# Performance work log

Hardware: AMD Instinct MI355X
Metric: run time of the kernel (lower is better)

The kernel has to match this reference:

```python
import jax, jax.numpy as jnp
import numpy as np

B, S, T = 32, 512, 64
DENC = 1024   # encoder dim == dhid
DHID = 1024
DEMB = 512
V = 32000
NEG = 1e20


def setup_inputs() -> dict:
    key = jax.random.key(0)
    ks = jax.random.split(key, 13)
    u = lambda k, shape, a: jax.random.uniform(k, shape, jnp.float32, -a, a)
    klstm = 1.0 / np.sqrt(DHID)
    kproj = 1.0 / np.sqrt(DENC + DHID)
    return {
        "enc": jax.random.normal(ks[0], (B, S, DENC), jnp.float32),
        "inp_mask": jnp.ones((B, S), jnp.float32),
        "label": jax.random.randint(ks[1], (B, T), 0, V),
        "emb_w": jax.random.normal(ks[2], (V, DEMB), jnp.float32) * 0.02,
        "W_ih": u(ks[3], (4 * DHID, DENC + DEMB), klstm),
        "b_ih": u(ks[4], (4 * DHID,), klstm),
        "W_hh": u(ks[5], (4 * DHID, DHID), klstm),
        "b_hh": u(ks[6], (4 * DHID,), klstm),
        "proj_W": u(ks[7], (DEMB, DENC + DHID), kproj),
        "proj_b": u(ks[8], (DEMB,), kproj),
        "emb0": u(ks[9], (DEMB,), 0.1),
        "h0": u(ks[10], (DHID,), 0.1),
        "c0": u(ks[11], (DHID,), 0.1),
    }


def reference(enc, inp_mask, label, emb_w, W_ih, b_ih, W_hh, b_hh,
              proj_W, proj_b, emb0, h0, c0):
    batch = enc.shape[0]
    vocab = emb_w.shape[0]
    h = jnp.broadcast_to(h0, (batch, h0.shape[0]))
    c = jnp.broadcast_to(c0, (batch, c0.shape[0]))
    e = jnp.broadcast_to(emb0, (batch, emb0.shape[0]))
    neg_mask = (1.0 - inp_mask) * NEG  # [B, S]
    emb_T = jax.lax.stop_gradient(emb_w).T  # detached vocab projection

    def step(carry, label_t):
        h, c, e = carry
        # attention over encoder states keyed by h
        score = jnp.einsum('bsd,bd->bs', enc, h) - neg_mask
        attn = jax.nn.softmax(score, axis=1)
        ctx = jnp.einsum('bs,bsd->bd', attn, enc)  # [B, DENC]
        # LSTMCell (torch gate order: i, f, g, o)
        x = jnp.concatenate([ctx, e], axis=1)
        gates = x @ W_ih.T + b_ih + h @ W_hh.T + b_hh
        i, f, g, o = jnp.split(gates, 4, axis=1)
        c = jax.nn.sigmoid(f) * c + jax.nn.sigmoid(i) * jnp.tanh(g)
        h = jax.nn.sigmoid(o) * jnp.tanh(c)
        # project to embedding space, score against vocab
        p = jnp.concatenate([ctx, h], axis=1) @ proj_W.T + proj_b
        out = p @ emb_T  # [B, V]
        # teacher forcing: next input embedding from label
        word = jnp.clip(label_t, 0, vocab - 1)
        e = emb_w[word]
        return (h, c, e), out

    _, outs = jax.lax.scan(step, (h, c, e), label.T)  # outs: [T, B, V]
    return jnp.transpose(outs, (1, 0, 2))  # [B, T, V]
```

## Files before the change

kernel.cpp:

```cpp
#include <hip/hip_runtime.h>
#include <hip/hip_bf16.h>


#define B_   32
#define S_   512
#define T_   64
#define DENC 1024
#define DHID 1024
#define DEMB 512
#define V_   32000
#define KX   2560
#define KP   2048
#define NCH  32

using short8 = __attribute__((ext_vector_type(8))) short;
using f32x4  = __attribute__((ext_vector_type(4))) float;
typedef __hip_bfloat16 bf16;

__device__ __forceinline__ float sigmoidf_(float x) { return 1.0f / (1.0f + expf(-x)); }
__device__ __forceinline__ bf16 bhi(float x) { return __float2bfloat16(x); }
__device__ __forceinline__ bf16 blo(float x) {
    return __float2bfloat16(x - __bfloat162float(__float2bfloat16(x)));
}

#define MFMA(a, b, c) __builtin_amdgcn_mfma_f32_16x16x32_bf16((a), (b), (c), 0, 0, 0)
#define DOT4(a, b) fmaf((a).x, (b).x, fmaf((a).y, (b).y, fmaf((a).z, (b).z, (a).w * (b).w)))


__global__ void k_build_wg(const float* __restrict__ W_ih, const float* __restrict__ W_hh,
                           const float* __restrict__ b_ih, const float* __restrict__ b_hh,
                           bf16* __restrict__ Wh, bf16* __restrict__ Wl, float* __restrict__ bias) {
    int jp = blockIdx.x;
    int g = jp & 3, d = jp >> 2;
    int j = g * 1024 + d;
    const float* wi = W_ih + (size_t)j * 1536;
    const float* wh = W_hh + (size_t)j * 1024;
    bf16* dh = Wh + (size_t)jp * KX;
    bf16* dl = Wl + (size_t)jp * KX;
    for (int i = threadIdx.x; i < 1024; i += 256) { float v = wi[i];      dh[i] = bhi(v);        dl[i] = blo(v); }
    for (int i = threadIdx.x; i < 1024; i += 256) { float v = wh[i];      dh[1024+i] = bhi(v);   dl[1024+i] = blo(v); }
    for (int i = threadIdx.x; i < 512;  i += 256) { float v = wi[1024+i]; dh[2048+i] = bhi(v);   dl[2048+i] = blo(v); }
    if (threadIdx.x == 0) bias[jp] = b_ih[j] + b_hh[j];
}

__global__ void k_cvt(const float* __restrict__ src, bf16* __restrict__ dst, long n) {
    long i = (long)blockIdx.x * blockDim.x + threadIdx.x;
    long stride = (long)gridDim.x * blockDim.x;
    for (; i < n; i += stride) dst[i] = __float2bfloat16(src[i]);
}

__global__ void k_cvt_split(const float* __restrict__ src, bf16* __restrict__ dh,
                            bf16* __restrict__ dl, long n) {
    long i = (long)blockIdx.x * blockDim.x + threadIdx.x;
    long stride = (long)gridDim.x * blockDim.x;
    for (; i < n; i += stride) { float v = src[i]; dh[i] = bhi(v); dl[i] = blo(v); }
}

__global__ void k_init(const float* __restrict__ h0, const float* __restrict__ c0,
                       const float* __restrict__ emb0,
                       float* __restrict__ h, float* __restrict__ c,
                       bf16* __restrict__ Hh, bf16* __restrict__ Hl,
                       bf16* __restrict__ Xh_, bf16* __restrict__ Xl_) {
    int b = blockIdx.x;
    for (int d = threadIdx.x; d < 1024; d += 256) {
        float v = h0[d];
        h[b * 1024 + d] = v;
        c[b * 1024 + d] = c0[d];
        Hh[b * 1024 + d] = bhi(v);
        Hl[b * 1024 + d] = blo(v);
    }
    for (int d = threadIdx.x; d < 512; d += 256) {
        float v = emb0[d];
        Xh_[(size_t)b * KX + 2048 + d] = bhi(v);
        Xl_[(size_t)b * KX + 2048 + d] = blo(v);
    }
}


__global__ __launch_bounds__(256) void k_att(
    const float* __restrict__ enc, const float* __restrict__ mask,
    const float* __restrict__ h,
    bf16* __restrict__ Xh_, bf16* __restrict__ Xl_,
    const bf16* __restrict__ Hh, const bf16* __restrict__ Hl,
    const bf16* __restrict__ PWh, const bf16* __restrict__ PWl,
    const float* __restrict__ pb, const float* __restrict__ emb_w,
    const int* __restrict__ label,
    bf16* __restrict__ Ph, bf16* __restrict__ Pl,
    float* __restrict__ pml, float* __restrict__ pctx, int t)
{
    __shared__ float pr[4][32][17];
    __shared__ float lctx[4][1024];
    __shared__ float lm[4], ll[4];

    int bid = blockIdx.x;
    int tid = threadIdx.x, wave = tid >> 6, lane = tid & 63;

    if (bid < 32) {
        if (t == 0) return;
        int tp = t - 1;
        int nb = bid * 16;
        int ncol = nb + (lane & 15);
        int kc = wave * 512;
        const short* ah;
        const short* al;
        size_t astr, aoff;
        if (wave < 2) { ah = (const short*)Xh_; al = (const short*)Xl_; astr = KX;   aoff = kc; }
        else          { ah = (const short*)Hh;  al = (const short*)Hl;  astr = 1024; aoff = kc - 1024; }
        const short* wrh = (const short*)PWh + (size_t)ncol * KP + kc + (lane >> 4) * 8;
        const short* wrl = (const short*)PWl + (size_t)ncol * KP + kc + (lane >> 4) * 8;
        size_t arow0 = (size_t)(lane & 15) * astr + aoff + (lane >> 4) * 8;
        size_t arow1 = (size_t)((lane & 15) + 16) * astr + aoff + (lane >> 4) * 8;
        f32x4 acc0 = {0, 0, 0, 0}, acc1 = {0, 0, 0, 0};
#pragma unroll 4
        for (int kk = 0; kk < 16; ++kk) {
            int ko = kk * 32;
            short8 a0h = *(const short8*)(ah + arow0 + ko);
            short8 a1h = *(const short8*)(ah + arow1 + ko);
            short8 a0l = *(const short8*)(al + arow0 + ko);
            short8 a1l = *(const short8*)(al + arow1 + ko);
            short8 bh = *(const short8*)(wrh + ko);
            short8 bl = *(const short8*)(wrl + ko);
            acc0 = MFMA(a0h, bh, acc0); acc1 = MFMA(a1h, bh, acc1);
            acc0 = MFMA(a0h, bl, acc0); acc1 = MFMA(a1h, bl, acc1);
            acc0 = MFMA(a0l, bh, acc0); acc1 = MFMA(a1l, bh, acc1);
        }
#pragma unroll
        for (int r = 0; r < 4; ++r) {
            pr[wave][(lane >> 4) * 4 + r][lane & 15]      = acc0[r];
            pr[wave][16 + (lane >> 4) * 4 + r][lane & 15] = acc1[r];
        }
        __syncthreads();
        for (int p = tid; p < 512; p += 256) {
            int bb = p >> 4, col = p & 15;
            float v = pr[0][bb][col] + pr[1][bb][col] + pr[2][bb][col] + pr[3][bb][col]
                      + pb[nb + col];
            size_t mi = (size_t)(bb * 64 + tp) * 512 + nb + col;
            Ph[mi] = bhi(v);
            Pl[mi] = blo(v);
        }
        int b = bid;
        int wd = label[b * 64 + tp];
        wd = wd < 0 ? 0 : (wd > V_ - 1 ? V_ - 1 : wd);
        const float* ew = emb_w + (size_t)wd * 512;
        for (int d = tid; d < 512; d += 256) {
            float v = ew[d];
            Xh_[(size_t)b * KX + 2048 + d] = bhi(v);
            Xl_[(size_t)b * KX + 2048 + d] = blo(v);
        }
        return;
    }

    if (t >= T_) return;
    int ab = bid - 32;
    int b = ab >> 5, ch = ab & (NCH - 1);

    float4 hreg[4];
    const float4* h4p = (const float4*)(h + b * 1024);
#pragma unroll
    for (int j = 0; j < 4; ++j) hreg[j] = h4p[j * 64 + lane];

    const float* encb = enc + (size_t)b * S_ * DENC;
    int srow0 = ch * 16 + wave * 4;
    const float4* r0 = (const float4*)(encb + (size_t)(srow0 + 0) * DENC);
    const float4* r1 = (const float4*)(encb + (size_t)(srow0 + 1) * DENC);
    const float4* r2 = (const float4*)(encb + (size_t)(srow0 + 2) * DENC);
    const float4* r3 = (const float4*)(encb + (size_t)(srow0 + 3) * DENC);
    float4 e00 = r0[lane], e01 = r0[64+lane], e02 = r0[128+lane], e03 = r0[192+lane];
    float4 e10 = r1[lane], e11 = r1[64+lane], e12 = r1[128+lane], e13 = r1[192+lane];
    float4 e20 = r2[lane], e21 = r2[64+lane], e22 = r2[128+lane], e23 = r2[192+lane];
    float4 e30 = r3[lane], e31 = r3[64+lane], e32 = r3[128+lane], e33 = r3[192+lane];

    float d0 = DOT4(e00,hreg[0]) + DOT4(e01,hreg[1]) + DOT4(e02,hreg[2]) + DOT4(e03,hreg[3]);
    float d1 = DOT4(e10,hreg[0]) + DOT4(e11,hreg[1]) + DOT4(e12,hreg[2]) + DOT4(e13,hreg[3]);
    float d2 = DOT4(e20,hreg[0]) + DOT4(e21,hreg[1]) + DOT4(e22,hreg[2]) + DOT4(e23,hreg[3]);
    float d3 = DOT4(e30,hreg[0]) + DOT4(e31,hreg[1]) + DOT4(e32,hreg[2]) + DOT4(e33,hreg[3]);
#pragma unroll
    for (int off = 32; off; off >>= 1) {
        d0 += __shfl_xor(d0, off, 64);
        d1 += __shfl_xor(d1, off, 64);
        d2 += __shfl_xor(d2, off, 64);
        d3 += __shfl_xor(d3, off, 64);
    }
    float sc0 = d0 - (1.0f - mask[b * S_ + srow0 + 0]) * 1e20f;
    float sc1 = d1 - (1.0f - mask[b * S_ + srow0 + 1]) * 1e20f;
    float sc2 = d2 - (1.0f - mask[b * S_ + srow0 + 2]) * 1e20f;
    float sc3 = d3 - (1.0f - mask[b * S_ + srow0 + 3]) * 1e20f;
    float mw = fmaxf(fmaxf(sc0, sc1), fmaxf(sc2, sc3));
    float w0 = expf(sc0 - mw), w1 = expf(sc1 - mw);
    float w2 = expf(sc2 - mw), w3 = expf(sc3 - mw);
    float lw = w0 + w1 + w2 + w3;
    float4 c0, c1, c2, c3;
    c0.x = w0*e00.x + w1*e10.x + w2*e20.x + w3*e30.x;
    c0.y = w0*e00.y + w1*e10.y + w2*e20.y + w3*e30.y;
    c0.z = w0*e00.z + w1*e10.z + w2*e20.z + w3*e30.z;
    c0.w = w0*e00.w + w1*e10.w + w2*e20.w + w3*e30.w;
    c1.x = w0*e01.x + w1*e11.x + w2*e21.x + w3*e31.x;
    c1.y = w0*e01.y + w1*e11.y + w2*e21.y + w3*e31.y;
    c1.z = w0*e01.z + w1*e11.z + w2*e21.z + w3*e31.z;
    c1.w = w0*e01.w + w1*e11.w + w2*e21.w + w3*e31.w;
    c2.x = w0*e02.x + w1*e12.x + w2*e22.x + w3*e32.x;
    c2.y = w0*e02.y + w1*e12.y + w2*e22.y + w3*e32.y;
    c2.z = w0*e02.z + w1*e12.z + w2*e22.z + w3*e32.z;
    c2.w = w0*e02.w + w1*e12.w + w2*e22.w + w3*e32.w;
    c3.x = w0*e03.x + w1*e13.x + w2*e23.x + w3*e33.x;
    c3.y = w0*e03.y + w1*e13.y + w2*e23.y + w3*e33.y;
    c3.z = w0*e03.z + w1*e13.z + w2*e23.z + w3*e33.z;
    c3.w = w0*e03.w + w1*e13.w + w2*e23.w + w3*e33.w;

    ((float4*)lctx[wave])[0 * 64 + lane] = c0;
    ((float4*)lctx[wave])[1 * 64 + lane] = c1;
    ((float4*)lctx[wave])[2 * 64 + lane] = c2;
    ((float4*)lctx[wave])[3 * 64 + lane] = c3;
    if (lane == 0) { lm[wave] = mw; ll[wave] = lw; }
    __syncthreads();

    float mb_ = fmaxf(fmaxf(lm[0], lm[1]), fmaxf(lm[2], lm[3]));
    float q0 = expf(lm[0] - mb_), q1 = expf(lm[1] - mb_);
    float q2 = expf(lm[2] - mb_), q3 = expf(lm[3] - mb_);
    float lb = ll[0] * q0 + ll[1] * q1 + ll[2] * q2 + ll[3] * q3;
    float4 a0 = ((float4*)lctx[0])[tid], a1 = ((float4*)lctx[1])[tid];
    float4 a2 = ((float4*)lctx[2])[tid], a3 = ((float4*)lctx[3])[tid];
    float4 v;
    v.x = a0.x * q0 + a1.x * q1 + a2.x * q2 + a3.x * q3;
    v.y = a0.y * q0 + a1.y * q1 + a2.y * q2 + a3.y * q3;
    v.z = a0.z * q0 + a1.z * q1 + a2.z * q2 + a3.z * q3;
    v.w = a0.w * q0 + a1.w * q1 + a2.w * q2 + a3.w * q3;
    int pi = b * NCH + ch;
    ((float4*)(pctx + (size_t)pi * 1024))[tid] = v;
    if (tid == 0) { pml[pi * 2] = mb_; pml[pi * 2 + 1] = lb; }
}


__global__ __launch_bounds__(256) void k_comb(const float* __restrict__ pml,
                                              const float* __restrict__ pctx,
                                              const bf16* __restrict__ Hh,
                                              const bf16* __restrict__ Hl,
                                              bf16* __restrict__ Xh_, bf16* __restrict__ Xl_) {
    __shared__ float sml[NCH * 2];
    __shared__ float wch[NCH];
    int b = blockIdx.x, tid = threadIdx.x;
    if (tid < NCH * 2) sml[tid] = pml[b * NCH * 2 + tid];
    __syncthreads();
    float mf = -3.0e38f;
#pragma unroll
    for (int c = 0; c < NCH; ++c) mf = fmaxf(mf, sml[2 * c]);
    float lt = 0.f;
#pragma unroll
    for (int c = 0; c < NCH; ++c) lt += sml[2 * c + 1] * expf(sml[2 * c] - mf);
    if (tid < NCH) wch[tid] = expf(sml[2 * tid] - mf);
    __syncthreads();
    float inv = 1.0f / lt;
    const float4* base = (const float4*)(pctx + (size_t)b * NCH * 1024) + tid;
    float4 sacc = {0, 0, 0, 0};
#pragma unroll 8
    for (int c = 0; c < NCH; ++c) {
        float wc = wch[c];
        float4 p = base[c * 256];
        sacc.x = fmaf(wc, p.x, sacc.x); sacc.y = fmaf(wc, p.y, sacc.y);
        sacc.z = fmaf(wc, p.z, sacc.z); sacc.w = fmaf(wc, p.w, sacc.w);
    }
    sacc.x *= inv; sacc.y *= inv; sacc.z *= inv; sacc.w *= inv;
    size_t xi = (size_t)b * KX + tid * 4;
    Xh_[xi + 0] = bhi(sacc.x); Xl_[xi + 0] = blo(sacc.x);
    Xh_[xi + 1] = bhi(sacc.y); Xl_[xi + 1] = blo(sacc.y);
    Xh_[xi + 2] = bhi(sacc.z); Xl_[xi + 2] = blo(sacc.z);
    Xh_[xi + 3] = bhi(sacc.w); Xl_[xi + 3] = blo(sacc.w);
    ((unsigned long long*)(Xh_ + (size_t)b * KX + 1024))[tid] =
        ((const unsigned long long*)(Hh + (size_t)b * 1024))[tid];
    ((unsigned long long*)(Xl_ + (size_t)b * KX + 1024))[tid] =
        ((const unsigned long long*)(Hl + (size_t)b * 1024))[tid];
}


__global__ __launch_bounds__(256) void k_gates(
    const bf16* __restrict__ Xh_, const bf16* __restrict__ Xl_,
    const bf16* __restrict__ Wh_, const bf16* __restrict__ Wl_,
    const float* __restrict__ bias,
    float* __restrict__ c, float* __restrict__ h,
    bf16* __restrict__ Hh, bf16* __restrict__ Hl)
{
    __shared__ float pr[4][32][17];
    int jb = blockIdx.x * 16;
    int tid = threadIdx.x, wave = tid >> 6, lane = tid & 63;
    int jcol = jb + (lane & 15);
    int kc = wave * 640 + (lane >> 4) * 8;
    const short* xhp = (const short*)Xh_ + kc;
    const short* xlp = (const short*)Xl_ + kc;
    const short* wrh = (const short*)Wh_ + (size_t)jcol * KX + kc;
    const short* wrl = (const short*)Wl_ + (size_t)jcol * KX + kc;
    size_t arow0 = (size_t)(lane & 15) * KX;
    size_t arow1 = (size_t)((lane & 15) + 16) * KX;
    f32x4 acc0 = {0, 0, 0, 0}, acc1 = {0, 0, 0, 0};
#pragma unroll 4
    for (int kk = 0; kk < 20; ++kk) {
        int ko = kk * 32;
        short8 a0h = *(const short8*)(xhp + arow0 + ko);
        short8 a1h = *(const short8*)(xhp + arow1 + ko);
        short8 a0l = *(const short8*)(xlp + arow0 + ko);
        short8 a1l = *(const short8*)(xlp + arow1 + ko);
        short8 bh = *(const short8*)(wrh + ko);
        short8 bl = *(const short8*)(wrl + ko);
        acc0 = MFMA(a0h, bh, acc0); acc1 = MFMA(a1h, bh, acc1);
        acc0 = MFMA(a0h, bl, acc0); acc1 = MFMA(a1h, bl, acc1);
        acc0 = MFMA(a0l, bh, acc0); acc1 = MFMA(a1l, bh, acc1);
    }
#pragma unroll
    for (int r = 0; r < 4; ++r) {
        pr[wave][(lane >> 4) * 4 + r][lane & 15]      = acc0[r];
        pr[wave][16 + (lane >> 4) * 4 + r][lane & 15] = acc1[r];
    }
    __syncthreads();
    if (tid < 128) {
        int bb = tid & 31, dd = tid >> 5;
        int cb = dd * 4;
        float gi = pr[0][bb][cb+0] + pr[1][bb][cb+0] + pr[2][bb][cb+0] + pr[3][bb][cb+0] + bias[jb+cb+0];
        float gf = pr[0][bb][cb+1] + pr[1][bb][cb+1] + pr[2][bb][cb+1] + pr[3][bb][cb+1] + bias[jb+cb+1];
        float gg = pr[0][bb][cb+2] + pr[1][bb][cb+2] + pr[2][bb][cb+2] + pr[3][bb][cb+2] + bias[jb+cb+2];
        float go = pr[0][bb][cb+3] + pr[1][bb][cb+3] + pr[2][bb][cb+3] + pr[3][bb][cb+3] + bias[jb+cb+3];
        int d = (jb >> 2) + dd;
        float cv = c[bb * 1024 + d];
        float cn = sigmoidf_(gf) * cv + sigmoidf_(gi) * tanhf(gg);
        float hn = sigmoidf_(go) * tanhf(cn);
        c[bb * 1024 + d] = cn;
        h[bb * 1024 + d] = hn;
        Hh[bb * 1024 + d] = bhi(hn);
        Hl[bb * 1024 + d] = blo(hn);
    }
}


__global__ __launch_bounds__(256) void k_out(const bf16* __restrict__ Ph,
                                             const bf16* __restrict__ Pl,
                                             const bf16* __restrict__ Eb,
                                             float* __restrict__ out) {
    int bid = blockIdx.x;
    int xcd = bid & 7, idx = bid >> 3;
    int vb_grp = xcd * 63 + (idx >> 5);
    if (vb_grp >= 500) return;
    int vb = vb_grp * 64;
    int mb = (idx & 31) * 64;

    __shared__ __align__(16) short ps[64][268];
    int tid = threadIdx.x, wave = tid >> 6, lane = tid & 63;
    int wr = (wave >> 1) * 32, wc = (wave & 1) * 32;
    f32x4 acc[2][2] = {{{0, 0, 0, 0}, {0, 0, 0, 0}}, {{0, 0, 0, 0}, {0, 0, 0, 0}}};
    const short* e0p = (const short*)Eb + (size_t)(vb + wc + (lane & 15)) * 512 + (lane >> 4) * 8;
    const short* e1p = e0p + 16 * 512;
    int srow = tid >> 5, scol = (tid & 31) * 8;

    short8 sr[8];
#pragma unroll
    for (int j = 0; j < 8; ++j)
        sr[j] = *(const short8*)((const short*)Ph + (size_t)(mb + srow + j * 8) * 512 + scol);

    short8 br0[8], br1[8];
    for (int ph = 0; ph < 4; ++ph) {
        int q = ph >> 1;
        if ((ph & 1) == 0) {
#pragma unroll
            for (int kk = 0; kk < 8; ++kk) {
                br0[kk] = *(const short8*)(e0p + q * 256 + kk * 32);
                br1[kk] = *(const short8*)(e1p + q * 256 + kk * 32);
            }
        }
        __syncthreads();
#pragma unroll
        for (int j = 0; j < 8; ++j)
            *(short8*)&ps[srow + j * 8][scol] = sr[j];
        __syncthreads();
        if (ph < 3) {
            int nq = (ph + 1) >> 1;
            const short* nsrc = ((ph + 1) & 1) ? (const short*)Pl : (const short*)Ph;
#pragma unroll
            for (int j = 0; j < 8; ++j)
                sr[j] = *(const short8*)(nsrc + (size_t)(mb + srow + j * 8) * 512 + nq * 256 + scol);
        }
#pragma unroll
        for (int kk = 0; kk < 8; ++kk) {
            int kcol = kk * 32 + (lane >> 4) * 8;
            short8 a0 = *(const short8*)(&ps[wr + (lane & 15)][kcol]);
            short8 a1 = *(const short8*)(&ps[wr + 16 + (lane & 15)][kcol]);
            acc[0][0] = MFMA(a0, br0[kk], acc[0][0]);
            acc[0][1] = MFMA(a0, br1[kk], acc[0][1]);
            acc[1][0] = MFMA(a1, br0[kk], acc[1][0]);
            acc[1][1] = MFMA(a1, br1[kk], acc[1][1]);
        }
    }
#pragma unroll
    for (int f0 = 0; f0 < 2; ++f0)
#pragma unroll
        for (int f1 = 0; f1 < 2; ++f1)
#pragma unroll
            for (int r = 0; r < 4; ++r) {
                int mm = mb + wr + 16 * f0 + (lane >> 4) * 4 + r;
                int vv = vb + wc + 16 * f1 + (lane & 15);
                __builtin_nontemporal_store(acc[f0][f1][r], &out[(size_t)mm * V_ + vv]);
            }
}


extern "C" void kernel_launch(void* const* d_in, const int* in_sizes, int n_in,
                              void* d_out, int out_size, void* d_ws, size_t ws_size,
                              hipStream_t stream) {
    (void)in_sizes; (void)n_in; (void)out_size; (void)ws_size;
    const float* enc    = (const float*)d_in[0];
    const float* mask   = (const float*)d_in[1];
    const int*   label  = (const int*)d_in[2];
    const float* emb_w  = (const float*)d_in[3];
    const float* W_ih   = (const float*)d_in[4];
    const float* b_ih   = (const float*)d_in[5];
    const float* W_hh   = (const float*)d_in[6];
    const float* b_hh   = (const float*)d_in[7];
    const float* proj_W = (const float*)d_in[8];
    const float* proj_b = (const float*)d_in[9];
    const float* emb0   = (const float*)d_in[10];
    const float* h0     = (const float*)d_in[11];
    const float* c0     = (const float*)d_in[12];
    float* out = (float*)d_out;

    char* w = (char*)d_ws;
    size_t o = 0;
    bf16* Wgh  = (bf16*)(w + o); o += (size_t)4096 * KX * 2;
    bf16* Wgl  = (bf16*)(w + o); o += (size_t)4096 * KX * 2;
    bf16* PWh  = (bf16*)(w + o); o += (size_t)512 * KP * 2;
    bf16* PWl  = (bf16*)(w + o); o += (size_t)512 * KP * 2;
    bf16* Eb   = (bf16*)(w + o); o += (size_t)V_ * 512 * 2;
    float* bias= (float*)(w + o); o += 4096 * 4;
    bf16* Xh   = (bf16*)(w + o); o += (size_t)32 * KX * 2;
    bf16* Xl   = (bf16*)(w + o); o += (size_t)32 * KX * 2;
    bf16* Hh   = (bf16*)(w + o); o += (size_t)32 * 1024 * 2;
    bf16* Hl   = (bf16*)(w + o); o += (size_t)32 * 1024 * 2;
    bf16* Ph   = (bf16*)(w + o); o += (size_t)2048 * 512 * 2;
    bf16* Pl   = (bf16*)(w + o); o += (size_t)2048 * 512 * 2;
    float* hb  = (float*)(w + o); o += (size_t)32 * 1024 * 4;
    float* cb  = (float*)(w + o); o += (size_t)32 * 1024 * 4;
    float* pml = (float*)(w + o); o += (size_t)32 * NCH * 2 * 4;
    float* pctx= (float*)(w + o); o += (size_t)32 * NCH * 1024 * 4;

    k_build_wg<<<4096, 256, 0, stream>>>(W_ih, W_hh, b_ih, b_hh, Wgh, Wgl, bias);
    k_cvt_split<<<1024, 256, 0, stream>>>(proj_W, PWh, PWl, (long)512 * KP);
    k_cvt<<<8192, 256, 0, stream>>>(emb_w, Eb, (long)V_ * 512);
    k_init<<<32, 256, 0, stream>>>(h0, c0, emb0, hb, cb, Hh, Hl, Xh, Xl);

    for (int t = 0; t <= T_; ++t) {
        k_att<<<32 + 32 * NCH, 256, 0, stream>>>(enc, mask, hb, Xh, Xl, Hh, Hl,
                                                 PWh, PWl, proj_b, emb_w, label,
                                                 Ph, Pl, pml, pctx, t);
        if (t < T_) {
            k_comb<<<32, 256, 0, stream>>>(pml, pctx, Hh, Hl, Xh, Xl);
            k_gates<<<256, 256, 0, stream>>>(Xh, Xl, Wgh, Wgl, bias, cb, hb, Hh, Hl);
        }
    }
    k_out<<<16128, 256, 0, stream>>>(Ph, Pl, Eb, out);
}
```

Measured before the change: 3.497 ms.

## Retile vocab-projection GEMM to 128x128 blocks with K-stepped LDS staging

Rewrites the final output GEMM kernel to use 128x128 output tiles per block, with each wave computing 64x64. It stages A-high, A-low and the embedding operand through LDS in K-chunks of 32, where the old kernel loaded B fragments directly from global memory per 64x64 tile. The aim is more MFMA work per byte loaded and fewer blocks, cutting global traffic on the embedding table. The change drops the XCD-aware block remapping and adds a barrier per K-step with no prefetch, so load latency may be exposed. Register pressure also rises with 16 accumulators.

```diff
diff --git a/kernel.cpp b/kernel.cpp
--- a/kernel.cpp
+++ b/kernel.cpp
@@ -334,67 +334,65 @@
                                              const bf16* __restrict__ Eb,
                                              float* __restrict__ out) {
     int bid = blockIdx.x;
-    int xcd = bid & 7, idx = bid >> 3;
-    int vb_grp = xcd * 63 + (idx >> 5);
-    if (vb_grp >= 500) return;
-    int vb = vb_grp * 64;
-    int mb = (idx & 31) * 64;
-
-    __shared__ __align__(16) short ps[64][268];
+    int vb = (bid >> 4) * 128;
+    int mb = (bid & 15) * 128;
+
+    __shared__ __align__(16) short Ah[128][36];
+    __shared__ __align__(16) short Al[128][36];
+    __shared__ __align__(16) short Bs[128][36];
+
     int tid = threadIdx.x, wave = tid >> 6, lane = tid & 63;
-    int wr = (wave >> 1) * 32, wc = (wave & 1) * 32;
-    f32x4 acc[2][2] = {{{0, 0, 0, 0}, {0, 0, 0, 0}}, {{0, 0, 0, 0}, {0, 0, 0, 0}}};
-    const short* e0p = (const short*)Eb + (size_t)(vb + wc + (lane & 15)) * 512 + (lane >> 4) * 8;
-    const short* e1p = e0p + 16 * 512;
-    int srow = tid >> 5, scol = (tid & 31) * 8;
-
-    short8 sr[8];
-#pragma unroll
-    for (int j = 0; j < 8; ++j)
-        sr[j] = *(const short8*)((const short*)Ph + (size_t)(mb + srow + j * 8) * 512 + scol);
-
-    short8 br0[8], br1[8];
-    for (int ph = 0; ph < 4; ++ph) {
-        int q = ph >> 1;
-        if ((ph & 1) == 0) {
-#pragma unroll
-            for (int kk = 0; kk < 8; ++kk) {
-                br0[kk] = *(const short8*)(e0p + q * 256 + kk * 32);
-                br1[kk] = *(const short8*)(e1p + q * 256 + kk * 32);
+    int wr = (wave >> 1) * 64, wc = (wave & 1) * 64;
+    int fr = lane & 15, kg = lane >> 4;
+
+    f32x4 acc[4][4];
+#pragma unroll
+    for (int m = 0; m < 4; ++m)
+#pragma unroll
+        for (int n = 0; n < 4; ++n) acc[m][n] = (f32x4){0, 0, 0, 0};
+
+    const short* Pp = (const short*)Ph;
+    const short* Plp = (const short*)Pl;
+    const short* Ep = (const short*)Eb;
+
+    for (int ks = 0; ks < 16; ++ks) {
+        int k0 = ks * 32;
+        __syncthreads();
+#pragma unroll
+        for (int j = 0; j < 2; ++j) {
+            int cch = tid + j * 256;
+            int r = cch >> 2, cg = (cch & 3) * 8;
+            *(short8*)&Ah[r][cg] = *(const short8*)(Pp  + (size_t)(mb + r) * 512 + k0 + cg);
+            *(short8*)&Al[r][cg] = *(const short8*)(Plp + (size_t)(mb + r) * 512 + k0 + cg);
+            *(short8*)&Bs[r][cg] = *(const short8*)(Ep  + (size_t)(vb + r) * 512 + k0 + cg);
+        }
+        __syncthreads();
+        short8 afh[4], afl[4], bf_[4];
+#pragma unroll
+        for (int m = 0; m < 4; ++m) {
+            afh[m] = *(const short8*)&Ah[wr + m * 16 + fr][kg * 8];
+            afl[m] = *(const short8*)&Al[wr + m * 16 + fr][kg * 8];
+        }
+#pragma unroll
+        for (int n = 0; n < 4; ++n)
+            bf_[n] = *(const short8*)&Bs[wc + n * 16 + fr][kg * 8];
+#pragma unroll
+        for (int m = 0; m < 4; ++m)
+#pragma unroll
+            for (int n = 0; n < 4; ++n) {
+                acc[m][n] = MFMA(afh[m], bf_[n], acc[m][n]);
+                acc[m][n] = MFMA(afl[m], bf_[n], acc[m][n]);
             }
-        }
-        __syncthreads();
-#pragma unroll
-        for (int j = 0; j < 8; ++j)
-            *(short8*)&ps[srow + j * 8][scol] = sr[j];
-        __syncthreads();
-        if (ph < 3) {
-            int nq = (ph + 1) >> 1;
-            const short* nsrc = ((ph + 1) & 1) ? (const short*)Pl : (const short*)Ph;
-#pragma unroll
-            for (int j = 0; j < 8; ++j)
-                sr[j] = *(const short8*)(nsrc + (size_t)(mb + srow + j * 8) * 512 + nq * 256 + scol);
-        }
-#pragma unroll
-        for (int kk = 0; kk < 8; ++kk) {
-            int kcol = kk * 32 + (lane >> 4) * 8;
-            short8 a0 = *(const short8*)(&ps[wr + (lane & 15)][kcol]);
-            short8 a1 = *(const short8*)(&ps[wr + 16 + (lane & 15)][kcol]);
-            acc[0][0] = MFMA(a0, br0[kk], acc[0][0]);
-            acc[0][1] = MFMA(a0, br1[kk], acc[0][1]);
-            acc[1][0] = MFMA(a1, br0[kk], acc[1][0]);
-            acc[1][1] = MFMA(a1, br1[kk], acc[1][1]);
-        }
-    }
-#pragma unroll
-    for (int f0 = 0; f0 < 2; ++f0)
-#pragma unroll
-        for (int f1 = 0; f1 < 2; ++f1)
+    }
+#pragma unroll
+    for (int m = 0; m < 4; ++m)
+#pragma unroll
+        for (int n = 0; n < 4; ++n)
 #pragma unroll
             for (int r = 0; r < 4; ++r) {
-                int mm = mb + wr + 16 * f0 + (lane >> 4) * 4 + r;
-                int vv = vb + wc + 16 * f1 + (lane & 15);
-                __builtin_nontemporal_store(acc[f0][f1][r], &out[(size_t)mm * V_ + vv]);
+                int mm = mb + wr + m * 16 + kg * 4 + r;
+                int vv = vb + wc + n * 16 + fr;
+                __builtin_nontemporal_store(acc[m][n][r], &out[(size_t)mm * V_ + vv]);
             }
 }
 
@@ -451,5 +449,5 @@
             k_gates<<<256, 256, 0, stream>>>(Xh, Xl, Wgh, Wgl, bias, cb, hb, Hh, Hl);
         }
     }
-    k_out<<<16128, 256, 0, stream>>>(Ph, Pl, Eb, out);
-}
+    k_out<<<4000, 256, 0, stream>>>(Ph, Pl, Eb, out);
+}
```

Result: faster. 3.334 ms (-4.7%).
